# Optimization experiments

Hardware: AMD Instinct MI355X
Metric: run time of the kernel (lower is better)

The kernel has to match this reference:

```python
import jax, jax.numpy as jnp
import numpy as np

B, S, DM, H = 2, 2048, 1024, 16        # dim_model = d_model//2 = 1024
WINDOW, DILATION, N_GLOBAL = 513, 2, 32
HD = DM // H
NEG = -1e9


def build_mask(n, window_size, dilation, global_idx):
    # dilated local window: |i-j| <= (window//2)*dilation and (i-j) % dilation == 0
    i = jnp.arange(n)[:, None]
    j = jnp.arange(n)[None, :]
    d = j - i
    half = window_size // 2
    local = (jnp.abs(d) <= half * dilation) & (jnp.mod(d, dilation) == 0)
    g = jnp.zeros((n,), bool).at[global_idx].set(True)
    # symmetric global token mask: global rows and columns fully attend
    return local | g[:, None] | g[None, :]


def setup_inputs() -> dict:
    key = jax.random.key(0)
    ks = jax.random.split(key, 9)
    std = 0.02
    inp = {
        "q": jax.random.normal(ks[0], (B, S, DM), jnp.float32),
        "k": jax.random.normal(ks[1], (B, S, DM), jnp.float32),
        "v": jax.random.normal(ks[2], (B, S, DM), jnp.float32),
        "Wq": jax.random.normal(ks[3], (DM, DM), jnp.float32) * std,
        "Wk": jax.random.normal(ks[4], (DM, DM), jnp.float32) * std,
        "Wv": jax.random.normal(ks[5], (DM, DM), jnp.float32) * std,
        "Wo": jax.random.normal(ks[6], (DM, DM), jnp.float32) * std,
        "bq": jnp.zeros((DM,), jnp.float32),
        "bk": jnp.zeros((DM,), jnp.float32),
        "bv": jnp.zeros((DM,), jnp.float32),
        "bo": jnp.zeros((DM,), jnp.float32),
        "global_idx": jax.random.randint(ks[7], (N_GLOBAL,), 0, S, jnp.int64)
        if jax.config.jax_enable_x64 else jax.random.randint(ks[7], (N_GLOBAL,), 0, S, jnp.int32),
    }
    return inp


def reference(q, k, v, Wq, Wk, Wv, Wo, bq, bk, bv, bo, global_idx):
    def split(x):  # [B,S,DM] -> [B,H,S,HD]
        return x.reshape(B, S, H, HD).transpose(0, 2, 1, 3)

    qh = split(q @ Wq.T + bq)
    kh = split(k @ Wk.T + bk)
    vh = split(v @ Wv.T + bv)

    scores = jnp.einsum("bhqd,bhkd->bhqk", qh, kh) / jnp.sqrt(jnp.asarray(HD, qh.dtype))
    mask = build_mask(S, WINDOW, DILATION, global_idx)  # [S,S] bool
    scores = jnp.where(mask[None, None], scores, NEG)
    attn = jax.nn.softmax(scores, axis=-1)
    out = jnp.einsum("bhqk,bhkd->bhqd", attn, vh)
    out = out.transpose(0, 2, 1, 3).reshape(B, S, DM)
    return out @ Wo.T + bo
```

## Files before the change

kernel.cpp:

```cpp
#include <hip/hip_runtime.h>
#include <hip/hip_bf16.h>
#include <math.h>

#define BB 2
#define SS 2048
#define DMM 1024
#define HH 16
#define HDD 64
#define NGLOB 32
#define MM 4096
#define SCALE2 0.18033688f

typedef __attribute__((ext_vector_type(8))) short short8;
typedef __attribute__((ext_vector_type(4))) float float4v;

__device__ __forceinline__ short f2bf(float f) {
    union { float f; unsigned u; } x; x.f = f;
    unsigned r = (x.u + 0x7fffu + ((x.u >> 16) & 1u)) >> 16;
    return (short)r;
}

#define ASYNC16(gp, lp) __builtin_amdgcn_global_load_lds( \
    (__attribute__((address_space(1))) void*)(gp), \
    (__attribute__((address_space(3))) void*)(lp), 16, 0, 0)

#define VSL(dim, key) ((dim) * 40 + (((((key) >> 3) ^ (((dim) >> 3) & 3)) << 3) | ((key) & 7)))

__global__ __launch_bounds__(256)
void convert_all(const float* __restrict__ q, const float* __restrict__ k,
                 const float* __restrict__ v,
                 const float* __restrict__ w0, const float* __restrict__ w1,
                 const float* __restrict__ w2, const float* __restrict__ w3,
                 short* __restrict__ abf, short* __restrict__ wbf,
                 const int* __restrict__ gidx, int* __restrict__ g,
                 int* __restrict__ glist, int* __restrict__ gcount) {
    int z = blockIdx.y;
    int t = threadIdx.x;
    if (z == 7) {
        if (blockIdx.x != 0) return;
        for (int i = t; i < SS; i += 256) g[i] = 0;
        if (t == 0) *gcount = 0;
        __syncthreads();
        if (t < NGLOB) {
            int j = gidx[t];
            if (j >= 0 && j < SS) g[j] = 1;
        }
        __syncthreads();
        for (int j = t; j < SS; j += 256) {
            if (g[j]) {
                int p = atomicAdd(gcount, 1);
                glist[p] = j;
            }
        }
        return;
    }
    const float* src;
    short* dst;
    size_t n;
    if (z < 3) {
        src = (z == 0) ? q : (z == 1) ? k : v;
        dst = abf + (size_t)z * ((size_t)MM * DMM);
        n = (size_t)MM * DMM;
    } else {
        int y = z - 3;
        src = (y == 0) ? w0 : (y == 1) ? w1 : (y == 2) ? w2 : w3;
        dst = wbf + (size_t)y * ((size_t)DMM * DMM);
        n = (size_t)DMM * DMM;
    }
    size_t i = ((size_t)blockIdx.x * 256 + t) * 8;
    if (i >= n) return;
    float4 a = *(const float4*)(src + i);
    float4 b = *(const float4*)(src + i + 4);
    short8 s;
    s[0]=f2bf(a.x); s[1]=f2bf(a.y); s[2]=f2bf(a.z); s[3]=f2bf(a.w);
    s[4]=f2bf(b.x); s[5]=f2bf(b.y); s[6]=f2bf(b.z); s[7]=f2bf(b.w);
    *(short8*)(dst + i) = s;
}

template<int OBF, int HEADSPLIT>
__global__ __launch_bounds__(512, 2)
void gemm256(const short* __restrict__ Abase, const short* __restrict__ Wbase,
             const float* __restrict__ b0, const float* __restrict__ b1,
             const float* __restrict__ b2,
             void* __restrict__ O0p, void* __restrict__ O1p, void* __restrict__ O2p) {
    __shared__ short As[2][256 * 64];
    __shared__ short Ws[2][256 * 64];

    int t = threadIdx.x;
    int z = blockIdx.y;
    const short* A    = Abase + (size_t)z * ((size_t)MM * DMM);
    const short* W    = Wbase + (size_t)z * ((size_t)DMM * DMM);
    const float* bias = (z == 0) ? b0 : (z == 1) ? b1 : b2;
    void* outp        = (z == 0) ? O0p : (z == 1) ? O1p : O2p;

    int bid = blockIdx.x;
    int mt = bid & 15, nt = bid >> 4;
    int m0 = mt * 256, n0 = nt * 256;

    int lane = t & 63, w = t >> 6;
    int quad = lane >> 4, col = lane & 15;
    int wm = (w >> 2) * 128;
    int wn = (w & 3) * 64;

    float4v acc[8][4];
    #pragma unroll
    for (int i = 0; i < 8; i++)
        #pragma unroll
        for (int j = 0; j < 4; j++) acc[i][j] = (float4v){0, 0, 0, 0};

    int srow = t >> 3;
    int scol = ((t & 7) ^ (srow & 7)) * 8;
    const short* Ap = A + (size_t)(m0 + srow) * DMM + scol;
    const short* Wp = W + (size_t)(n0 + srow) * DMM + scol;

    #define ST_W(bf, tt, h) ASYNC16(Wp + (size_t)(h) * 64 * DMM + (size_t)(tt) * 64, \
                                    &Ws[bf][(h) * 4096 + t * 8])
    #define ST_A(bf, tt, h) ASYNC16(Ap + (size_t)(h) * 64 * DMM + (size_t)(tt) * 64, \
                                    &As[bf][(h) * 4096 + t * 8])

    int c7 = col & 7;

    ST_W(0, 0, 0); ST_W(0, 0, 1); ST_W(0, 0, 2); ST_W(0, 0, 3);
    ST_A(0, 0, 0); ST_A(0, 0, 2); ST_A(0, 0, 1); ST_A(0, 0, 3);
    asm volatile("s_waitcnt vmcnt(2)" ::: "memory");
    __builtin_amdgcn_s_barrier();

    for (int it = 0; it < 16; it++) {
        int cur = it & 1, nb = cur ^ 1;
        bool pf = (it < 15);

        short8 bF[4][2];
        #pragma unroll
        for (int j = 0; j < 4; j++) {
            int rB = (wn + 16 * j + col) * 64;
            #pragma unroll
            for (int ks = 0; ks < 2; ks++)
                bF[j][ks] = *(short8*)&Ws[cur][rB + ((((ks << 2) | quad) ^ c7) << 3)];
        }

        #pragma unroll
        for (int p = 0; p < 4; p++) {
            short8 aF[2][2];
            #pragma unroll
            for (int u = 0; u < 2; u++) {
                int rA = (wm + 16 * (2 * p + u) + col) * 64;
                #pragma unroll
                for (int ks = 0; ks < 2; ks++)
                    aF[u][ks] = *(short8*)&As[cur][rA + ((((ks << 2) | quad) ^ c7) << 3)];
            }
            if (pf) {
                if (p == 0)      { ST_W(nb, it + 1, 0); ST_W(nb, it + 1, 1); }
                else if (p == 1) { ST_W(nb, it + 1, 2); ST_W(nb, it + 1, 3); }
                else if (p == 2) { ST_A(nb, it + 1, 0); ST_A(nb, it + 1, 2); }
                else             { ST_A(nb, it + 1, 1); ST_A(nb, it + 1, 3); }
            }
            __builtin_amdgcn_s_barrier();
            __builtin_amdgcn_s_setprio(1);
            #pragma unroll
            for (int ks = 0; ks < 2; ks++)
                #pragma unroll
                for (int u = 0; u < 2; u++)
                    #pragma unroll
                    for (int j = 0; j < 4; j++)
                        acc[2 * p + u][j] = __builtin_amdgcn_mfma_f32_16x16x32_bf16(
                            aF[u][ks], bF[j][ks], acc[2 * p + u][j], 0, 0, 0);
            __builtin_amdgcn_s_setprio(0);
            if (p == 1) {
                if (pf) asm volatile("s_waitcnt vmcnt(4)" ::: "memory");
                else    asm volatile("s_waitcnt vmcnt(0)" ::: "memory");
            }
            if (p == 3 && pf)
                asm volatile("s_waitcnt vmcnt(2)" ::: "memory");
            __builtin_amdgcn_s_barrier();
        }
    }
    #undef ST_W
    #undef ST_A

    #pragma unroll
    for (int i = 0; i < 8; i++) {
        #pragma unroll
        for (int j = 0; j < 4; j++) {
            int n = n0 + wn + 16 * j + col;
            float bn = bias[n];
            #pragma unroll
            for (int r = 0; r < 4; r++) {
                int m = m0 + wm + 16 * i + quad * 4 + r;
                float val = acc[i][j][r] + bn;
                size_t idx;
                if (HEADSPLIT) {
                    int b = m >> 11;
                    int s = m & 2047;
                    int h = n >> 6;
                    int hd = n & 63;
                    idx = (((size_t)b * HH + h) * SS + s) * HDD + hd;
                } else {
                    idx = (size_t)m * DMM + n;
                }
                if (OBF) ((short*)outp)[idx] = f2bf(val);
                else     ((float*)outp)[idx] = val;
            }
        }
    }
}

__global__ __launch_bounds__(512, 2)
void gemm128wo(const short* __restrict__ A, const short* __restrict__ W,
               const float* __restrict__ bias, float* __restrict__ out) {
    __shared__ short As[2][128 * 64];
    __shared__ short Ws[2][128 * 64];

    int t = threadIdx.x;
    int bid = blockIdx.x;
    int mt = bid & 31, nt = bid >> 5;
    int m0 = mt * 128, n0 = nt * 128;

    int lane = t & 63, w = t >> 6;
    int quad = lane >> 4, col = lane & 15;
    int wm = (w >> 2) * 64;
    int wn = (w & 3) * 32;

    float4v acc[4][2];
    #pragma unroll
    for (int i = 0; i < 4; i++)
        #pragma unroll
        for (int j = 0; j < 2; j++) acc[i][j] = (float4v){0, 0, 0, 0};

    int srow = t >> 3;
    int scol = ((t & 7) ^ (srow & 7)) * 8;
    const short* Ap = A + (size_t)(m0 + srow) * DMM + scol;
    const short* Wp = W + (size_t)(n0 + srow) * DMM + scol;

    #define STAGEWO(bf, tt) do { size_t kk = (size_t)(tt) * 64; \
        ASYNC16(Ap + kk,                      &As[bf][t * 8]); \
        ASYNC16(Ap + 64 * (size_t)DMM + kk,   &As[bf][4096 + t * 8]); \
        ASYNC16(Wp + kk,                      &Ws[bf][t * 8]); \
        ASYNC16(Wp + 64 * (size_t)DMM + kk,   &Ws[bf][4096 + t * 8]); \
    } while (0)

    int c7 = col & 7;

    STAGEWO(0, 0);

    for (int it = 0; it < 16; it++) {
        int cur = it & 1;
        if (it < 15) {
            STAGEWO(cur ^ 1, it + 1);
            asm volatile("s_waitcnt vmcnt(4)" ::: "memory");
        } else {
            asm volatile("s_waitcnt vmcnt(0)" ::: "memory");
        }
        __builtin_amdgcn_s_barrier();

        short8 bF[2][2];
        #pragma unroll
        for (int j = 0; j < 2; j++) {
            int rB = (wn + 16 * j + col) * 64;
            #pragma unroll
            for (int ks = 0; ks < 2; ks++)
                bF[j][ks] = *(short8*)&Ws[cur][rB + ((((ks << 2) | quad) ^ c7) << 3)];
        }

        #pragma unroll
        for (int p = 0; p < 2; p++) {
            if (p) __builtin_amdgcn_s_barrier();
            short8 aF[2][2];
            #pragma unroll
            for (int u = 0; u < 2; u++) {
                int rA = (wm + 16 * (2 * p + u) + col) * 64;
                #pragma unroll
                for (int ks = 0; ks < 2; ks++)
                    aF[u][ks] = *(short8*)&As[cur][rA + ((((ks << 2) | quad) ^ c7) << 3)];
            }
            __builtin_amdgcn_s_setprio(1);
            #pragma unroll
            for (int ks = 0; ks < 2; ks++)
                #pragma unroll
                for (int u = 0; u < 2; u++)
                    #pragma unroll
                    for (int j = 0; j < 2; j++)
                        acc[2 * p + u][j] = __builtin_amdgcn_mfma_f32_16x16x32_bf16(
                            aF[u][ks], bF[j][ks], acc[2 * p + u][j], 0, 0, 0);
            __builtin_amdgcn_s_setprio(0);
        }
        __builtin_amdgcn_s_barrier();
    }
    #undef STAGEWO

    #pragma unroll
    for (int i = 0; i < 4; i++) {
        #pragma unroll
        for (int j = 0; j < 2; j++) {
            int n = n0 + wn + 16 * j + col;
            float bn = bias[n];
            #pragma unroll
            for (int r = 0; r < 4; r++) {
                int m = m0 + wm + 16 * i + quad * 4 + r;
                out[(size_t)m * DMM + n] = acc[i][j][r] + bn;
            }
        }
    }
}

__global__ __launch_bounds__(256)
void attn_fused(const short* __restrict__ qh, const short* __restrict__ kh,
                const short* __restrict__ vh, const int* __restrict__ glist,
                const int* __restrict__ gcount, short* __restrict__ ao,
                float* __restrict__ pl, float* __restrict__ pO) {
    __shared__ __align__(16) char smem[29184];
    int t = threadIdx.x;
    int bid = blockIdx.x;
    int nG = *gcount;

    if (bid < 1024) {
        short* Qs = (short*)smem;
        short* Ks = Qs + 64 * 72;
        short* Vt = Ks + 32 * 72;
        short* Ps = Vt + 64 * 40;
        int*   gjs = (int*)(Ps + 4 * 16 * 40);

        int xcd = bid & 7, idx = bid >> 3;
        int gl  = idx >> 4;
        int qt  = idx & 15;
        int gid = xcd * 8 + gl;
        int z   = gid >> 4;
        int h   = gid & 15;
        int b = z >> 1, p = z & 1;
        int qq0 = qt * 64;

        const short* Qb = qh + ((size_t)(b * HH + h) * SS) * HDD;
        const short* Kb = kh + ((size_t)(b * HH + h) * SS) * HDD;
        const short* Vb = vh + ((size_t)(b * HH + h) * SS) * HDD;

        int row8 = t >> 3;
        int dim8 = (t & 7) * 8;

        #pragma unroll
        for (int rr = 0; rr < 2; rr++) {
            int row = rr * 32 + row8;
            int i = 2 * (qq0 + row) + p;
            short8 qv = *(const short8*)(Qb + (size_t)i * HDD + dim8);
            *(short8*)&Qs[row * 72 + dim8] = qv;
        }
        if (t < 32) gjs[t] = (t < nG) ? glist[t] : -1000000;
        __syncthreads();

        int lane = t & 63, w = t >> 6;
        int quad = lane >> 4, col = lane & 15;

        short8 qf0 = *(short8*)&Qs[(16 * w + col) * 72 + quad * 8];
        short8 qf1 = *(short8*)&Qs[(16 * w + col) * 72 + 32 + quad * 8];

        float4v O0 = {0,0,0,0}, O1 = {0,0,0,0}, O2 = {0,0,0,0}, O3 = {0,0,0,0};
        float lst[4] = {0.f, 0.f, 0.f, 0.f};

        short8 kvP, vvP, kvN, vvN;
        {
            int srow = 2 * (qq0 - 256 + row8) + p;
            srow = srow < 0 ? 0 : (srow > SS - 1 ? SS - 1 : srow);
            kvP = *(const short8*)(Kb + (size_t)srow * HDD + dim8);
            vvP = *(const short8*)(Vb + (size_t)srow * HDD + dim8);
        }

        for (int c = 0; c < 19; c++) {
            __syncthreads();
            *(short8*)&Ks[row8 * 72 + dim8] = kvP;
            #pragma unroll
            for (int j = 0; j < 8; j++) {
                int d = dim8 + j;
                Vt[VSL(d, row8)] = vvP[j];
            }
            if (c < 18) {
                int cn = c + 1;
                int ch0n = qq0 - 256 + cn * 32;
                int srow;
                if (cn < 18) srow = 2 * (ch0n + row8) + p;
                else         srow = (row8 < nG) ? gjs[row8] : 0;
                srow = srow < 0 ? 0 : (srow > SS - 1 ? SS - 1 : srow);
                kvN = *(const short8*)(Kb + (size_t)srow * HDD + dim8);
                vvN = *(const short8*)(Vb + (size_t)srow * HDD + dim8);
            }
            __syncthreads();

            int ch0 = qq0 - 256 + c * 32;

            short8 kA0 = *(short8*)&Ks[col * 72 + quad * 8];
            short8 kA1 = *(short8*)&Ks[col * 72 + 32 + quad * 8];
            short8 kB0 = *(short8*)&Ks[(16 + col) * 72 + quad * 8];
            short8 kB1 = *(short8*)&Ks[(16 + col) * 72 + 32 + quad * 8];
            float4v sA = {0,0,0,0}, sB = {0,0,0,0};
            sA = __builtin_amdgcn_mfma_f32_16x16x32_bf16(qf0, kA0, sA, 0, 0, 0);
            sA = __builtin_amdgcn_mfma_f32_16x16x32_bf16(qf1, kA1, sA, 0, 0, 0);
            sB = __builtin_amdgcn_mfma_f32_16x16x32_bf16(qf0, kB0, sB, 0, 0, 0);
            sB = __builtin_amdgcn_mfma_f32_16x16x32_bf16(qf1, kB1, sB, 0, 0, 0);

            if (c < 18) {
                int nlo = -ch0;
                int nhi = 1023 - ch0;
                #pragma unroll
                for (int r = 0; r < 4; r++) {
                    int qq = qq0 + 16 * w + quad * 4 + r;
                    int u  = qq - ch0;
                    int lo = max(u - 256, nlo);
                    int hi = min(u + 256, nhi);
                    bool vA = (col >= lo) && (col <= hi);
                    bool vB = (col + 16 >= lo) && (col + 16 <= hi);
                    float pa = vA ? exp2f(sA[r] * SCALE2) : 0.f;
                    float pb = vB ? exp2f(sB[r] * SCALE2) : 0.f;
                    lst[r] += pa + pb;
                    Ps[(w * 16 + quad * 4 + r) * 40 + col]      = f2bf(pa);
                    Ps[(w * 16 + quad * 4 + r) * 40 + col + 16] = f2bf(pb);
                }
            } else {
                #pragma unroll
                for (int r = 0; r < 4; r++) {
                    int qq = qq0 + 16 * w + quad * 4 + r;
                    int i = 2 * qq + p;
                    int jA = gjs[col], jB = gjs[col + 16];
                    int dA = jA - i, dB = jB - i;
                    int aA = dA < 0 ? -dA : dA;
                    int aB = dB < 0 ? -dB : dB;
                    bool vA = (jA >= 0) && !((aA <= 512) && ((dA & 1) == 0));
                    bool vB = (jB >= 0) && !((aB <= 512) && ((dB & 1) == 0));
                    float pa = vA ? exp2f(sA[r] * SCALE2) : 0.f;
                    float pb = vB ? exp2f(sB[r] * SCALE2) : 0.f;
                    lst[r] += pa + pb;
                    Ps[(w * 16 + quad * 4 + r) * 40 + col]      = f2bf(pa);
                    Ps[(w * 16 + quad * 4 + r) * 40 + col + 16] = f2bf(pb);
                }
            }
            asm volatile("s_waitcnt lgkmcnt(0)" ::: "memory");

            short8 pf  = *(short8*)&Ps[(w * 16 + col) * 40 + quad * 8];
            short8 vf0 = *(short8*)&Vt[(col) * 40 + ((quad ^ ((col >> 3) & 3)) << 3)];
            short8 vf1 = *(short8*)&Vt[(16 + col) * 40 + ((quad ^ (((16 + col) >> 3) & 3)) << 3)];
            short8 vf2 = *(short8*)&Vt[(32 + col) * 40 + ((quad ^ (((32 + col) >> 3) & 3)) << 3)];
            short8 vf3 = *(short8*)&Vt[(48 + col) * 40 + ((quad ^ (((48 + col) >> 3) & 3)) << 3)];
            O0 = __builtin_amdgcn_mfma_f32_16x16x32_bf16(pf, vf0, O0, 0, 0, 0);
            O1 = __builtin_amdgcn_mfma_f32_16x16x32_bf16(pf, vf1, O1, 0, 0, 0);
            O2 = __builtin_amdgcn_mfma_f32_16x16x32_bf16(pf, vf2, O2, 0, 0, 0);
            O3 = __builtin_amdgcn_mfma_f32_16x16x32_bf16(pf, vf3, O3, 0, 0, 0);

            kvP = kvN; vvP = vvN;
        }

        #pragma unroll
        for (int r = 0; r < 4; r++) {
            float l = lst[r];
            #pragma unroll
            for (int mk = 1; mk < 16; mk <<= 1) l += __shfl_xor(l, mk);
            float inv = 1.0f / l;
            int q = 16 * w + quad * 4 + r;
            int i = 2 * (qq0 + q) + p;
            short* dst = ao + ((size_t)b * SS + i) * DMM + h * HDD;
            dst[col]      = f2bf(O0[r] * inv);
            dst[col + 16] = f2bf(O1[r] * inv);
            dst[col + 32] = f2bf(O2[r] * inv);
            dst[col + 48] = f2bf(O3[r] * inv);
        }
    } else {
        short* Qs  = (short*)smem;
        short* Ksf = Qs + 32 * 72;
        short* Vtf = Ksf + 2 * 32 * 72;
        short* Ps  = Vtf + 2 * 64 * 40;

        int r0 = bid - 1024;
        int s = r0 & 7, h = (r0 >> 3) & 15, b = r0 >> 7;

        const short* Qb = qh + ((size_t)(b * HH + h) * SS) * HDD;
        const short* Kb = kh + ((size_t)(b * HH + h) * SS) * HDD;
        const short* Vb = vh + ((size_t)(b * HH + h) * SS) * HDD;

        int row8 = t >> 3, dim8 = (t & 7) * 8;
        {
            int cq = row8 < nG ? row8 : 0;
            int src = glist[cq];
            short8 qv = *(const short8*)(Qb + (size_t)src * HDD + dim8);
            *(short8*)&Qs[row8 * 72 + dim8] = qv;
        }
        __syncthreads();

        int lane = t & 63, w = t >> 6;
        int quad = lane >> 4, col = lane & 15;
        int g = w >> 1, qt = w & 1;

        short8 qf0 = *(short8*)&Qs[(qt * 16 + col) * 72 + quad * 8];
        short8 qf1 = *(short8*)&Qs[(qt * 16 + col) * 72 + 32 + quad * 8];

        float4v O0 = {0,0,0,0}, O1 = {0,0,0,0}, O2 = {0,0,0,0}, O3 = {0,0,0,0};
        float lst[4] = {0.f, 0.f, 0.f, 0.f};

        int js0 = s * 256;
        for (int it = 0; it < 4; it++) {
            __syncthreads();
            int r64 = t >> 2, dimb = (t & 3) * 16;
            int j = js0 + it * 64 + r64;
            const short* kp = Kb + (size_t)j * HDD + dimb;
            const short* vp = Vb + (size_t)j * HDD + dimb;
            short8 k0 = *(const short8*)kp, k1 = *(const short8*)(kp + 8);
            short8 v0 = *(const short8*)vp, v1 = *(const short8*)(vp + 8);
            int half = r64 >> 5, r32 = r64 & 31;
            short* Ksh = Ksf + half * (32 * 72);
            short* Vth = Vtf + half * (64 * 40);
            *(short8*)&Ksh[r32 * 72 + dimb]     = k0;
            *(short8*)&Ksh[r32 * 72 + dimb + 8] = k1;
            #pragma unroll
            for (int u = 0; u < 8; u++) {
                int d = dimb + u;
                Vth[VSL(d, r32)] = v0[u];
            }
            #pragma unroll
            for (int u = 0; u < 8; u++) {
                int d = dimb + 8 + u;
                Vth[VSL(d, r32)] = v1[u];
            }
            __syncthreads();

            short* Ksg = Ksf + g * (32 * 72);
            short* Vtg = Vtf + g * (64 * 40);
            short8 kA0 = *(short8*)&Ksg[col * 72 + quad * 8];
            short8 kA1 = *(short8*)&Ksg[col * 72 + 32 + quad * 8];
            short8 kB0 = *(short8*)&Ksg[(16 + col) * 72 + quad * 8];
            short8 kB1 = *(short8*)&Ksg[(16 + col) * 72 + 32 + quad * 8];
            float4v sA = {0,0,0,0}, sB = {0,0,0,0};
            sA = __builtin_amdgcn_mfma_f32_16x16x32_bf16(qf0, kA0, sA, 0, 0, 0);
            sA = __builtin_amdgcn_mfma_f32_16x16x32_bf16(qf1, kA1, sA, 0, 0, 0);
            sB = __builtin_amdgcn_mfma_f32_16x16x32_bf16(qf0, kB0, sB, 0, 0, 0);
            sB = __builtin_amdgcn_mfma_f32_16x16x32_bf16(qf1, kB1, sB, 0, 0, 0);

            #pragma unroll
            for (int r = 0; r < 4; r++) {
                float pa = exp2f(sA[r] * SCALE2);
                float pb = exp2f(sB[r] * SCALE2);
                lst[r] += pa + pb;
                Ps[(w * 16 + quad * 4 + r) * 40 + col]      = f2bf(pa);
                Ps[(w * 16 + quad * 4 + r) * 40 + col + 16] = f2bf(pb);
            }
            asm volatile("s_waitcnt lgkmcnt(0)" ::: "memory");

            short8 pf  = *(short8*)&Ps[(w * 16 + col) * 40 + quad * 8];
            short8 vf0 = *(short8*)&Vtg[(col) * 40 + ((quad ^ ((col >> 3) & 3)) << 3)];
            short8 vf1 = *(short8*)&Vtg[(16 + col) * 40 + ((quad ^ (((16 + col) >> 3) & 3)) << 3)];
            short8 vf2 = *(short8*)&Vtg[(32 + col) * 40 + ((quad ^ (((32 + col) >> 3) & 3)) << 3)];
            short8 vf3 = *(short8*)&Vtg[(48 + col) * 40 + ((quad ^ (((48 + col) >> 3) & 3)) << 3)];
            O0 = __builtin_amdgcn_mfma_f32_16x16x32_bf16(pf, vf0, O0, 0, 0, 0);
            O1 = __builtin_amdgcn_mfma_f32_16x16x32_bf16(pf, vf1, O1, 0, 0, 0);
            O2 = __builtin_amdgcn_mfma_f32_16x16x32_bf16(pf, vf2, O2, 0, 0, 0);
            O3 = __builtin_amdgcn_mfma_f32_16x16x32_bf16(pf, vf3, O3, 0, 0, 0);
        }

        int sp = s * 2 + g;
        size_t base = ((size_t)(b * HH + h) * 16 + sp) * 32;
        #pragma unroll
        for (int r = 0; r < 4; r++) {
            float l = lst[r];
            #pragma unroll
            for (int mk = 1; mk < 16; mk <<= 1) l += __shfl_xor(l, mk);
            int q = qt * 16 + quad * 4 + r;
            if (col == 0) pl[base + q] = l;
            float* Od = pO + (base + q) * 64;
            Od[col]      = O0[r];
            Od[col + 16] = O1[r];
            Od[col + 32] = O2[r];
            Od[col + 48] = O3[r];
        }
    }
}

__global__ __launch_bounds__(256)
void global_merge(const float* __restrict__ pl, const float* __restrict__ pO,
                  const int* __restrict__ glist, const int* __restrict__ gcount,
                  short* __restrict__ ao) {
    int h = blockIdx.x, b = blockIdx.y;
    int t = threadIdx.x;
    int d = t & 63, qg = t >> 6;
    int nG = *gcount;
    size_t bh = ((size_t)(b * HH + h) * 16) * 32;

    for (int q = qg; q < nG; q += 4) {
        float L = 0.f, acc = 0.f;
        #pragma unroll
        for (int sp = 0; sp < 16; sp++) {
            L   += pl[bh + sp * 32 + q];
            acc += pO[(bh + sp * 32 + q) * 64 + d];
        }
        int i = glist[q];
        ao[((size_t)b * SS + i) * DMM + h * HDD + d] = f2bf(acc / L);
    }
}

extern "C" void kernel_launch(void* const* d_in, const int* in_sizes, int n_in,
                              void* d_out, int out_size, void* d_ws, size_t ws_size,
                              hipStream_t stream) {
    const float* q  = (const float*)d_in[0];
    const float* k  = (const float*)d_in[1];
    const float* v  = (const float*)d_in[2];
    const float* Wq = (const float*)d_in[3];
    const float* Wk = (const float*)d_in[4];
    const float* Wv = (const float*)d_in[5];
    const float* Wo = (const float*)d_in[6];
    const float* bq = (const float*)d_in[7];
    const float* bk = (const float*)d_in[8];
    const float* bv = (const float*)d_in[9];
    const float* bo = (const float*)d_in[10];
    const int* gidx = (const int*)d_in[11];
    float* out = (float*)d_out;

    const size_t NE = (size_t)BB * SS * DMM;
    const size_t WE = (size_t)DMM * DMM;
    int*   g      = (int*)d_ws;
    int*   glist  = g + SS;
    int*   gcount = glist + SS;
    short* qh     = (short*)((char*)d_ws + 32768);
    short* kh     = qh + NE;
    short* vh     = kh + NE;
    short* ao     = vh + NE;
    short* wbf    = ao + NE;
    short* wo     = wbf + 3 * WE;
    short* abf    = wbf + 4 * WE;
    float* pl     = (float*)abf;
    float* pO     = pl + 16384;

    dim3 gc(2048, 8);
    convert_all<<<gc, 256, 0, stream>>>(q, k, v, Wq, Wk, Wv, Wo, abf, wbf,
                                        gidx, g, glist, gcount);

    dim3 gq(64, 3);
    gemm256<1, 1><<<gq, 512, 0, stream>>>(abf, wbf, bq, bk, bv, qh, kh, vh);

    attn_fused<<<1280, 256, 0, stream>>>(qh, kh, vh, glist, gcount, ao, pl, pO);

    dim3 gm(HH, BB);
    global_merge<<<gm, 256, 0, stream>>>(pl, pO, glist, gcount, ao);

    gemm128wo<<<256, 512, 0, stream>>>(ao, wo, bo, out);
}
```

Measured before the change: 208.4 us.

## Fuse global-row merge into attention via last-block atomic counter; flatten convert grid

Removes the separate global_merge kernel: each global-row attention block increments a per-(batch,head) counter, and the eighth (last) arriving block merges the partial softmax sums and outputs into the attention output. Local blocks skip writing rows that are global, since the merge overwrites them, which avoids a write race now that both run in one kernel. The convert kernel is also flattened to a 1D grid with no wasted blocks (the old 2D grid launched many idle blocks for the weight slices). This saves a kernel launch and idle blocks, at the cost of threadfences, an atomic and a serialized tail merge done in one block per head.

```diff
diff --git a/kernel.cpp b/kernel.cpp
--- a/kernel.cpp
+++ b/kernel.cpp
@@ -27,19 +27,20 @@
 #define VSL(dim, key) ((dim) * 40 + (((((key) >> 3) ^ (((dim) >> 3) & 3)) << 3) | ((key) & 7)))
 
 __global__ __launch_bounds__(256)
-void convert_all(const float* __restrict__ q, const float* __restrict__ k,
-                 const float* __restrict__ v,
-                 const float* __restrict__ w0, const float* __restrict__ w1,
-                 const float* __restrict__ w2, const float* __restrict__ w3,
-                 short* __restrict__ abf, short* __restrict__ wbf,
-                 const int* __restrict__ gidx, int* __restrict__ g,
-                 int* __restrict__ glist, int* __restrict__ gcount) {
-    int z = blockIdx.y;
+void convert_flat(const float* __restrict__ q, const float* __restrict__ k,
+                  const float* __restrict__ v,
+                  const float* __restrict__ w0, const float* __restrict__ w1,
+                  const float* __restrict__ w2, const float* __restrict__ w3,
+                  short* __restrict__ abf, short* __restrict__ wbf,
+                  const int* __restrict__ gidx, int* __restrict__ g,
+                  int* __restrict__ glist, int* __restrict__ gcount,
+                  int* __restrict__ bcnt) {
+    int bid = blockIdx.x;
     int t = threadIdx.x;
-    if (z == 7) {
-        if (blockIdx.x != 0) return;
+    if (bid == 6144 + 2048) {
         for (int i = t; i < SS; i += 256) g[i] = 0;
         if (t == 0) *gcount = 0;
+        if (t < 32) bcnt[t] = 0;
         __syncthreads();
         if (t < NGLOB) {
             int j = gidx[t];
@@ -56,25 +57,23 @@
     }
     const float* src;
     short* dst;
-    size_t n;
-    if (z < 3) {
-        src = (z == 0) ? q : (z == 1) ? k : v;
-        dst = abf + (size_t)z * ((size_t)MM * DMM);
-        n = (size_t)MM * DMM;
+    if (bid < 6144) {
+        int z = bid >> 11;
+        size_t off = ((size_t)(bid & 2047) << 11) + (size_t)t * 8;
+        src = ((z == 0) ? q : (z == 1) ? k : v) + off;
+        dst = abf + ((size_t)z << 22) + off;
     } else {
-        int y = z - 3;
-        src = (y == 0) ? w0 : (y == 1) ? w1 : (y == 2) ? w2 : w3;
-        dst = wbf + (size_t)y * ((size_t)DMM * DMM);
-        n = (size_t)DMM * DMM;
+        int y = (bid - 6144) >> 9;
+        size_t off = ((size_t)((bid - 6144) & 511) << 11) + (size_t)t * 8;
+        src = ((y == 0) ? w0 : (y == 1) ? w1 : (y == 2) ? w2 : w3) + off;
+        dst = wbf + ((size_t)y << 20) + off;
     }
-    size_t i = ((size_t)blockIdx.x * 256 + t) * 8;
-    if (i >= n) return;
-    float4 a = *(const float4*)(src + i);
-    float4 b = *(const float4*)(src + i + 4);
+    float4 a = *(const float4*)(src);
+    float4 b = *(const float4*)(src + 4);
     short8 s;
     s[0]=f2bf(a.x); s[1]=f2bf(a.y); s[2]=f2bf(a.z); s[3]=f2bf(a.w);
     s[4]=f2bf(b.x); s[5]=f2bf(b.y); s[6]=f2bf(b.z); s[7]=f2bf(b.w);
-    *(short8*)(dst + i) = s;
+    *(short8*)dst = s;
 }
 
 template<int OBF, int HEADSPLIT>
@@ -305,9 +304,10 @@
 __global__ __launch_bounds__(256)
 void attn_fused(const short* __restrict__ qh, const short* __restrict__ kh,
                 const short* __restrict__ vh, const int* __restrict__ glist,
-                const int* __restrict__ gcount, short* __restrict__ ao,
-                float* __restrict__ pl, float* __restrict__ pO) {
-    __shared__ __align__(16) char smem[29184];
+                const int* __restrict__ gcount, const int* __restrict__ gmap,
+                short* __restrict__ ao, float* __restrict__ pl, float* __restrict__ pO,
+                int* __restrict__ bcnt) {
+    __shared__ __align__(16) char smem[29200];
     int t = threadIdx.x;
     int bid = blockIdx.x;
     int nG = *gcount;
@@ -452,17 +452,20 @@
             float inv = 1.0f / l;
             int q = 16 * w + quad * 4 + r;
             int i = 2 * (qq0 + q) + p;
-            short* dst = ao + ((size_t)b * SS + i) * DMM + h * HDD;
-            dst[col]      = f2bf(O0[r] * inv);
-            dst[col + 16] = f2bf(O1[r] * inv);
-            dst[col + 32] = f2bf(O2[r] * inv);
-            dst[col + 48] = f2bf(O3[r] * inv);
+            if (!gmap[i]) {
+                short* dst = ao + ((size_t)b * SS + i) * DMM + h * HDD;
+                dst[col]      = f2bf(O0[r] * inv);
+                dst[col + 16] = f2bf(O1[r] * inv);
+                dst[col + 32] = f2bf(O2[r] * inv);
+                dst[col + 48] = f2bf(O3[r] * inv);
+            }
         }
     } else {
         short* Qs  = (short*)smem;
         short* Ksf = Qs + 32 * 72;
         short* Vtf = Ksf + 2 * 32 * 72;
         short* Ps  = Vtf + 2 * 64 * 40;
+        int* sflag = (int*)(smem + 29184);
 
         int r0 = bid - 1024;
         int s = r0 & 7, h = (r0 >> 3) & 15, b = r0 >> 7;
@@ -564,28 +567,29 @@
             Od[col + 32] = O2[r];
             Od[col + 48] = O3[r];
         }
-    }
-}
-
-__global__ __launch_bounds__(256)
-void global_merge(const float* __restrict__ pl, const float* __restrict__ pO,
-                  const int* __restrict__ glist, const int* __restrict__ gcount,
-                  short* __restrict__ ao) {
-    int h = blockIdx.x, b = blockIdx.y;
-    int t = threadIdx.x;
-    int d = t & 63, qg = t >> 6;
-    int nG = *gcount;
-    size_t bh = ((size_t)(b * HH + h) * 16) * 32;
-
-    for (int q = qg; q < nG; q += 4) {
-        float L = 0.f, acc = 0.f;
-        #pragma unroll
-        for (int sp = 0; sp < 16; sp++) {
-            L   += pl[bh + sp * 32 + q];
-            acc += pO[(bh + sp * 32 + q) * 64 + d];
-        }
-        int i = glist[q];
-        ao[((size_t)b * SS + i) * DMM + h * HDD + d] = f2bf(acc / L);
+
+        __threadfence();
+        __syncthreads();
+        if (t == 0) {
+            int bh = b * HH + h;
+            *sflag = atomicAdd(&bcnt[bh], 1);
+        }
+        __syncthreads();
+        if (*sflag == 7) {
+            __threadfence();
+            int d = t & 63, qg = t >> 6;
+            size_t bh2 = ((size_t)(b * HH + h) * 16) * 32;
+            for (int q2 = qg; q2 < nG; q2 += 4) {
+                float L = 0.f, acc2 = 0.f;
+                #pragma unroll
+                for (int sp2 = 0; sp2 < 16; sp2++) {
+                    L    += pl[bh2 + sp2 * 32 + q2];
+                    acc2 += pO[(bh2 + sp2 * 32 + q2) * 64 + d];
+                }
+                int i = glist[q2];
+                ao[((size_t)b * SS + i) * DMM + h * HDD + d] = f2bf(acc2 / L);
+            }
+        }
     }
 }
 
@@ -611,6 +615,7 @@
     int*   g      = (int*)d_ws;
     int*   glist  = g + SS;
     int*   gcount = glist + SS;
+    int*   bcnt   = gcount + 1;
     short* qh     = (short*)((char*)d_ws + 32768);
     short* kh     = qh + NE;
     short* vh     = kh + NE;
@@ -621,17 +626,13 @@
     float* pl     = (float*)abf;
     float* pO     = pl + 16384;
 
-    dim3 gc(2048, 8);
-    convert_all<<<gc, 256, 0, stream>>>(q, k, v, Wq, Wk, Wv, Wo, abf, wbf,
-                                        gidx, g, glist, gcount);
+    convert_flat<<<8193, 256, 0, stream>>>(q, k, v, Wq, Wk, Wv, Wo, abf, wbf,
+                                           gidx, g, glist, gcount, bcnt);
 
     dim3 gq(64, 3);
     gemm256<1, 1><<<gq, 512, 0, stream>>>(abf, wbf, bq, bk, bv, qh, kh, vh);
 
-    attn_fused<<<1280, 256, 0, stream>>>(qh, kh, vh, glist, gcount, ao, pl, pO);
-
-    dim3 gm(HH, BB);
-    global_merge<<<gm, 256, 0, stream>>>(pl, pO, glist, gcount, ao);
+    attn_fused<<<1280, 256, 0, stream>>>(qh, kh, vh, glist, gcount, g, ao, pl, pO, bcnt);
 
     gemm128wo<<<256, 512, 0, stream>>>(ao, wo, bo, out);
 }
```

Result: slower. 254.8 us (+22.3%).
